# Kernel optimization log

Hardware: AMD Instinct MI355X
Metric: run time of the kernel (lower is better)

The kernel has to match this reference:

```python
import jax, jax.numpy as jnp
import numpy as np

B_J0 = 0.01   # baseline threshold
DT = 1.0
BETA = 1.8    # adaptation strength
LENS = 0.5
SCALE = 6.0
HIGHT = 0.15
GAMMA = 0.5


def _gauss(x, mu, sigma):
    return jnp.exp(-(x - mu) ** 2 / (2.0 * sigma ** 2)) / jnp.sqrt(2.0 * jnp.pi) / sigma


@jax.custom_vjp
def spike_fn(x):
    return (x > 0).astype(x.dtype)


def _spike_fwd(x):
    return spike_fn(x), x


def _spike_bwd(x, g):
    # multi-gaussian surrogate gradient (config.gradient_type == 'MG')
    temp = (_gauss(x, 0.0, LENS) * (1.0 + HIGHT)
            - _gauss(x, LENS, SCALE * LENS) * HIGHT
            - _gauss(x, -LENS, SCALE * LENS) * HIGHT)
    return (g * temp * GAMMA,)


spike_fn.defvjp(_spike_fwd, _spike_bwd)


def setup_inputs() -> dict:
    key = jax.random.key(0)
    ks = jax.random.split(key, 20)
    Bt, T, I, H, O = 256, 250, 700, 128, 20
    f32 = jnp.float32
    return {
        'x': jax.random.uniform(ks[0], (Bt, T, I), dtype=f32),
        'mask': jnp.ones((2, H, H), dtype=f32),
        'w_ih1': (jax.random.normal(ks[1], (I, H), dtype=f32) / np.sqrt(I).astype(np.float32)),
        'b_ih1': jnp.zeros((H,), f32),
        'w_h1h1': (jax.random.normal(ks[2], (H, H), dtype=f32) / np.sqrt(H).astype(np.float32)),
        'b_h1h1': jnp.zeros((H,), f32),
        'w_h1h2': (jax.random.normal(ks[3], (H, H), dtype=f32) / np.sqrt(H).astype(np.float32)),
        'b_h1h2': jnp.zeros((H,), f32),
        'w_h2h2': (jax.random.normal(ks[4], (H, H), dtype=f32) / np.sqrt(H).astype(np.float32)),
        'b_h2h2': jnp.zeros((H,), f32),
        'w_h2o': (jax.random.normal(ks[5], (H, O), dtype=f32) / np.sqrt(H).astype(np.float32)),
        'b_h2o': jnp.zeros((O,), f32),
        'tau_adp_h1': 150.0 + 10.0 * jax.random.normal(ks[6], (H,), dtype=f32),
        'tau_adp_h2': 150.0 + 10.0 * jax.random.normal(ks[7], (H,), dtype=f32),
        'tau_m_h1': 20.0 + 5.0 * jax.random.normal(ks[8], (H,), dtype=f32),
        'tau_m_h2': 20.0 + 5.0 * jax.random.normal(ks[9], (H,), dtype=f32),
        'tau_m_o': 20.0 + 5.0 * jax.random.normal(ks[10], (O,), dtype=f32),
        'hid1_mem0': jax.random.uniform(ks[11], (Bt, H), dtype=f32),
        'hid2_mem0': jax.random.uniform(ks[12], (Bt, H), dtype=f32),
        'out_mem0': jax.random.uniform(ks[13], (Bt, O), dtype=f32),
    }


def _forward(x, mask, w_ih1, b_ih1, w_h1h1, b_h1h1, w_h1h2, b_h1h2,
             w_h2h2, b_h2h2, w_h2o, b_h2o, tau_adp_h1, tau_adp_h2,
             tau_m_h1, tau_m_h2, tau_m_o, hid1_mem0, hid2_mem0, out_mem0):
    Bt, T, _ = x.shape
    H = w_ih1.shape[1]
    O = w_h2o.shape[1]
    # dropout mask applied to recurrent weights (weights stored [in, out])
    w11 = w_h1h1 * mask[0]
    w22 = w_h2h2 * mask[1]
    a1 = jnp.exp(-DT / tau_m_h1)
    r1 = jnp.exp(-DT / tau_adp_h1)
    a2 = jnp.exp(-DT / tau_m_h2)
    r2 = jnp.exp(-DT / tau_adp_h2)
    ao = jnp.exp(-DT / tau_m_o)
    # precompute input projection for all timesteps: [T, B, H]
    xin = jnp.einsum('bti,ih->tbh', x, w_ih1) + b_ih1

    def step(carry, inps):
        h1m, h1s, h2m, h2s, om, b1, b2, acc, s1, s2 = carry
        xt, t = inps
        # layer 1 (adaptive LIF)
        i1 = xt + h1s @ w11 + b_h1h1
        b1 = r1 * b1 + (1.0 - r1) * h1s
        B1 = B_J0 + BETA * b1
        h1m = h1m * a1 + (1.0 - a1) * i1 - B1 * h1s * DT
        h1s = spike_fn(h1m - B1)
        s1 = s1 + h1s
        # layer 2 (adaptive LIF)
        i2 = h1s @ w_h1h2 + b_h1h2 + h2s @ w22 + b_h2h2
        b2 = r2 * b2 + (1.0 - r2) * h2s
        B2 = B_J0 + BETA * b2
        h2m = h2m * a2 + (1.0 - a2) * i2 - B2 * h2s * DT
        h2s = spike_fn(h2m - B2)
        s2 = s2 + h2s
        # leaky-integrator readout (no spike)
        io = h2s @ w_h2o + b_h2o
        om = om * ao + (1.0 - ao) * io
        acc = acc + jnp.where(t > 10, jax.nn.softmax(om, axis=-1), 0.0)
        return (h1m, h1s, h2m, h2s, om, b1, b2, acc, s1, s2), None

    zH = jnp.zeros((Bt, H), x.dtype)
    carry0 = (hid1_mem0, zH, hid2_mem0, zH, out_mem0,
              jnp.full((Bt, H), B_J0, x.dtype), jnp.full((Bt, H), B_J0, x.dtype),
              jnp.zeros((Bt, O), x.dtype), zH, zH)
    carry, _ = jax.lax.scan(step, carry0, (xin, jnp.arange(T)))
    output, s1, s2 = carry[7], carry[8], carry[9]
    A_norm = jnp.sum(jnp.abs(w11)) + jnp.sum(jnp.abs(w22))
    return output, s1 / T, s2 / T, A_norm


def reference(x, mask, w_ih1, b_ih1, w_h1h1, b_h1h1, w_h1h2, b_h1h2,
              w_h2h2, b_h2h2, w_h2o, b_h2o, tau_adp_h1, tau_adp_h2,
              tau_m_h1, tau_m_h2, tau_m_o, hid1_mem0, hid2_mem0, out_mem0):
    return _forward(x, mask, w_ih1, b_ih1, w_h1h1, b_h1h1, w_h1h2, b_h1h2,
                    w_h2h2, b_h2h2, w_h2o, b_h2o, tau_adp_h1, tau_adp_h2,
                    tau_m_h1, tau_m_h2, tau_m_o, hid1_mem0, hid2_mem0, out_mem0)
```

## Files before the change

kernel.cpp:

```cpp
#include <hip/hip_runtime.h>
#include <math.h>

#define TT 250
#define BT 256
#define HN 128
#define ON 20
#define KIN 700
#define NKT 22

#define XIN_OFF 0
#define WPKH_OFF 8192000
#define WPKL_OFF 8237056

typedef __attribute__((ext_vector_type(8))) short bf16x8;
typedef __attribute__((ext_vector_type(4))) float f32x4;

__device__ __forceinline__ unsigned short bf16rne(float f) {
    unsigned u = __float_as_uint(f);
    unsigned r = u + 0x7fffu + ((u >> 16) & 1u);
    return (unsigned short)(r >> 16);
}
__device__ __forceinline__ void hilo(float v, short& h, short& l) {
    unsigned short hh = bf16rne(v);
    float vh = __uint_as_float((unsigned)hh << 16);
    h = (short)hh;
    l = (short)bf16rne(v - vh);
}

__device__ __forceinline__ void gl_lds16(const void* g, void* l) {
    __builtin_amdgcn_global_load_lds(
        (const __attribute__((address_space(1))) unsigned int*)g,
        (__attribute__((address_space(3))) unsigned int*)l, 16, 0, 0);
}

__global__ __launch_bounds__(256) void packw(const float* __restrict__ w,
                                             unsigned short* __restrict__ ph,
                                             unsigned short* __restrict__ pl) {
    int i = blockIdx.x * 256 + threadIdx.x;
    int k = i >> 7, c = i & 127;
    float v = (k < KIN) ? w[k * HN + c] : 0.f;
    short h, l;
    hilo(v, h, l);
    int dst = (((k >> 5) * 8 + (c >> 4)) * 64 + (((k >> 3) & 3) * 16 + (c & 15))) * 8 + (k & 7);
    ph[dst] = (unsigned short)h;
    pl[dst] = (unsigned short)l;
}

__device__ __forceinline__ void stage_kt(const unsigned short* __restrict__ wph,
                                         const unsigned short* __restrict__ wpl,
                                         void* buf, int kt, int tid) {
    const char* sh = (const char*)wph + kt * 8192 + tid * 16;
    const char* sl = (const char*)wpl + kt * 8192 + tid * 16;
    char* b = (char*)buf;
    const int wb = (tid >> 6) * 1024;
    gl_lds16(sh,        b + wb);
    gl_lds16(sh + 4096, b + wb + 4096);
    gl_lds16(sl,        b + wb + 8192);
    gl_lds16(sl + 4096, b + wb + 12288);
}

__device__ __forceinline__ void loadx8(float* av, const float* p, bool tailq3) {
    *(float4*)&av[0] = *(const float4*)p;
    if (tailq3) {
        av[4] = 0.f; av[5] = 0.f; av[6] = 0.f; av[7] = 0.f;
    } else {
        *(float4*)&av[4] = *(const float4*)(p + 4);
    }
}

__global__ __launch_bounds__(256, 2) void gemm_in(const float* __restrict__ x,
        const unsigned short* __restrict__ wph, const unsigned short* __restrict__ wpl,
        const float* __restrict__ bias1, const float* __restrict__ bias2,
        float* __restrict__ xin) {
    __shared__ __align__(16) unsigned char wbuf[2][16384];
    const int tid = threadIdx.x;
    const int w = tid >> 6, lane = tid & 63;
    const int q = lane >> 4, li = lane & 15;
    const long mbase = (long)blockIdx.x * 128;
    const float* xr0 = x + (mbase + w * 16 + li) * KIN + q * 8;

    f32x4 acc[2][8];
#pragma unroll
    for (int c = 0; c < 2; c++)
#pragma unroll
        for (int nt = 0; nt < 8; nt++) acc[c][nt] = (f32x4){0.f, 0.f, 0.f, 0.f};

    stage_kt(wph, wpl, wbuf[0], 0, tid);
    float av[2][8];
    loadx8(av[0], xr0, false);
    loadx8(av[1], xr0 + 64 * KIN, false);
    __syncthreads();

    for (int kt = 0; kt < NKT; kt++) {
        if (kt + 1 < NKT)
            stage_kt(wph, wpl, wbuf[(kt + 1) & 1], kt + 1, tid);
        const bf16x8* cv = (const bf16x8*)&wbuf[kt & 1][0];
#pragma unroll
        for (int c = 0; c < 2; c++) {
            bf16x8 ah, al;
#pragma unroll
            for (int j = 0; j < 8; j++) {
                short h, l;
                hilo(av[c][j], h, l);
                ah[j] = h; al[j] = l;
            }
            if (kt + 1 < NKT)
                loadx8(av[c], xr0 + c * (64 * KIN) + (kt + 1) * 32,
                       (kt + 1 == NKT - 1) && (q == 3));
#pragma unroll
            for (int nt = 0; nt < 8; nt++) {
                bf16x8 bh = cv[nt * 64 + lane];
                bf16x8 bl = cv[512 + nt * 64 + lane];
                acc[c][nt] = __builtin_amdgcn_mfma_f32_16x16x32_bf16(ah, bh, acc[c][nt], 0, 0, 0);
                acc[c][nt] = __builtin_amdgcn_mfma_f32_16x16x32_bf16(al, bh, acc[c][nt], 0, 0, 0);
                acc[c][nt] = __builtin_amdgcn_mfma_f32_16x16x32_bf16(ah, bl, acc[c][nt], 0, 0, 0);
            }
        }
        __syncthreads();
    }

    float b12[8];
#pragma unroll
    for (int nt = 0; nt < 8; nt++) {
        int c = nt * 16 + li;
        b12[nt] = bias1[c] + bias2[c];
    }
#pragma unroll
    for (int c = 0; c < 2; c++) {
#pragma unroll
        for (int r = 0; r < 4; r++) {
            long m = mbase + c * 64 + w * 16 + q * 4 + r;
            int bq = (int)(((unsigned long long)m * 67109ull) >> 24);
            int tt = (int)m - bq * 250;
            float* dst = xin + ((size_t)tt * BT + bq) * HN;
#pragma unroll
            for (int nt = 0; nt < 8; nt++) dst[nt * 16 + li] = acc[c][nt][r] + b12[nt];
        }
    }
}

__global__ __launch_bounds__(512, 2) void snn_scan(
    const float* __restrict__ xin, const float* __restrict__ mask,
    const float* __restrict__ w_h1h1, const float* __restrict__ w_h1h2,
    const float* __restrict__ b_h1h2, const float* __restrict__ w_h2h2,
    const float* __restrict__ b_h2h2, const float* __restrict__ w_h2o,
    const float* __restrict__ b_h2o, const float* __restrict__ tau_adp1,
    const float* __restrict__ tau_adp2, const float* __restrict__ taum1,
    const float* __restrict__ taum2, const float* __restrict__ taumo,
    const float* __restrict__ h1m0, const float* __restrict__ h2m0,
    const float* __restrict__ om0, float* __restrict__ out) {

    __shared__ __align__(16) unsigned short sA1[2 * 2048];
    __shared__ __align__(16) unsigned short sA2[2 * 2048];
    __shared__ float omb[2][16 * ON];
    __shared__ float red[8];

    const int tid = threadIdx.x;
    const int w = tid >> 6, lane = tid & 63;
    const int q = lane >> 4, li = lane & 15;
    const int col = w * 16 + li;
    const int r0 = blockIdx.x * 16;

    bf16x8 h11[4], l11[4], h22[4], l22[4], h12[4], l12[4], hO[4], lO[4];
    const int ocol = (w == 6) ? li : 16 + li;
    const bool oval = (w >= 6) && (ocol < ON);
    float pn = 0.f;
#pragma unroll
    for (int kt = 0; kt < 4; kt++) {
#pragma unroll
        for (int j = 0; j < 8; j++) {
            const int k = kt * 32 + q * 8 + j;
            const int idx = k * HN + col;
            float v11 = w_h1h1[idx] * mask[idx];
            float v22 = w_h2h2[idx] * mask[HN * HN + idx];
            float v12 = w_h1h2[idx];
            pn += fabsf(v11) + fabsf(v22);
            short hh, ll;
            hilo(v11, hh, ll); h11[kt][j] = hh; l11[kt][j] = ll;
            hilo(v22, hh, ll); h22[kt][j] = hh; l22[kt][j] = ll;
            hilo(v12, hh, ll); h12[kt][j] = hh; l12[kt][j] = ll;
            float vO = oval ? w_h2o[k * ON + ocol] : 0.f;
            hilo(vO, hh, ll); hO[kt][j] = hh; lO[kt][j] = ll;
        }
    }

    const float a1 = expf(-1.f / taum1[col]);
    const float r1 = expf(-1.f / tau_adp1[col]);
    const float a2 = expf(-1.f / taum2[col]);
    const float r2 = expf(-1.f / tau_adp2[col]);
    const float cc2 = b_h1h2[col] + b_h2h2[col];
    float h1m[4], h2m[4], b1[4], b2[4], c1[4], c2n[4];
    unsigned s1bits = 0, s2bits = 0;
#pragma unroll
    for (int r = 0; r < 4; r++) {
        h1m[r] = h1m0[(r0 + q * 4 + r) * HN + col];
        h2m[r] = h2m0[(r0 + q * 4 + r) * HN + col];
        b1[r] = 0.01f; b2[r] = 0.01f; c1[r] = 0.f; c2n[r] = 0.f;
    }
    const float ao = oval ? expf(-1.f / taumo[ocol]) : 0.f;
    const float bo = oval ? b_h2o[ocol] : 0.f;
    float om[4];
#pragma unroll
    for (int r = 0; r < 4; r++)
        om[r] = oval ? om0[(r0 + q * 4 + r) * ON + ocol] : 0.f;
    const int sm = lane >> 2, ob = (lane & 3) * 5;
    float accs[5] = {0.f, 0.f, 0.f, 0.f, 0.f};

    {
        unsigned* z1 = (unsigned*)sA1;
        unsigned* z2 = (unsigned*)sA2;
        z1[tid] = 0u; z1[tid + 512] = 0u; z1[tid + 1024] = 0u; z1[tid + 1536] = 0u;
        z2[tid] = 0u; z2[tid + 512] = 0u; z2[tid + 1024] = 0u; z2[tid + 1536] = 0u;
    }

#pragma unroll
    for (int off = 32; off > 0; off >>= 1) pn += __shfl_down(pn, off);
    if (lane == 0) red[w] = pn;
    __syncthreads();
    if (tid == 0 && blockIdx.x == 0) {
        float s = 0.f;
#pragma unroll
        for (int i = 0; i < 8; i++) s += red[i];
        out[70656] = s;
    }

    const int wbase = (w >> 1) * 512 + (((2 * w + (li >> 3)) & 3) * 16 + q * 4) * 8 + (li & 7);
    const unsigned short ONE = 0x3F80u;

    const float* xp = xin + (size_t)(r0 + q * 4) * HN + col;

    for (int i = 0; i < TT; i++) {
        const int pa = i & 1;

        float xt[4];
#pragma unroll
        for (int r = 0; r < 4; r++) xt[r] = xp[r * HN];
        xp += BT * HN;

        const bf16x8* g1p = (const bf16x8*)(sA1 + ((pa ^ 1) << 11));
        const bf16x8* f2p = (const bf16x8*)(sA2 + (pa << 11));
        bf16x8 g1[4], f2[4];
#pragma unroll
        for (int kt = 0; kt < 4; kt++) {
            g1[kt] = g1p[kt * 64 + lane];
            f2[kt] = f2p[kt * 64 + lane];
        }

        f32x4 aI = {0.f, 0.f, 0.f, 0.f}, aJ = {0.f, 0.f, 0.f, 0.f}, aG = {0.f, 0.f, 0.f, 0.f};
#pragma unroll
        for (int kt = 0; kt < 4; kt++) {
            aI = __builtin_amdgcn_mfma_f32_16x16x32_bf16(g1[kt], h11[kt], aI, 0, 0, 0);
            aI = __builtin_amdgcn_mfma_f32_16x16x32_bf16(g1[kt], l11[kt], aI, 0, 0, 0);
            aJ = __builtin_amdgcn_mfma_f32_16x16x32_bf16(g1[kt], h12[kt], aJ, 0, 0, 0);
            aJ = __builtin_amdgcn_mfma_f32_16x16x32_bf16(g1[kt], l12[kt], aJ, 0, 0, 0);
            aG = __builtin_amdgcn_mfma_f32_16x16x32_bf16(f2[kt], h22[kt], aG, 0, 0, 0);
            aG = __builtin_amdgcn_mfma_f32_16x16x32_bf16(f2[kt], l22[kt], aG, 0, 0, 0);
        }
        f32x4 aO = {0.f, 0.f, 0.f, 0.f};
        if (w >= 6) {
#pragma unroll
            for (int kt = 0; kt < 4; kt++) {
                aO = __builtin_amdgcn_mfma_f32_16x16x32_bf16(f2[kt], hO[kt], aO, 0, 0, 0);
                aO = __builtin_amdgcn_mfma_f32_16x16x32_bf16(f2[kt], lO[kt], aO, 0, 0, 0);
            }
        }

        if (i >= 1) {
            unsigned short* s2w = sA2 + ((pa ^ 1) << 11);
#pragma unroll
            for (int r = 0; r < 4; r++) {
                const float sv = (float)((s2bits >> r) & 1u);
                const float i2 = aJ[r] + aG[r] + cc2;
                b2[r] = r2 * b2[r] + (1.f - r2) * sv;
                const float B = 0.01f + 1.8f * b2[r];
                h2m[r] = a2 * h2m[r] + (1.f - a2) * i2 - B * sv;
                const bool sp = (h2m[r] - B) > 0.f;
                s2bits = sp ? (s2bits | (1u << r)) : (s2bits & ~(1u << r));
                c2n[r] += sp ? 1.f : 0.f;
                s2w[wbase + r * 8] = sp ? ONE : (unsigned short)0;
            }
        }

        if (w >= 6 && i >= 2) {
#pragma unroll
            for (int r = 0; r < 4; r++) {
                om[r] = ao * om[r] + (1.f - ao) * (bo + aO[r]);
                if (oval) omb[pa][(q * 4 + r) * ON + ocol] = om[r];
            }
        }

        if (w == 0 && i >= 14) {
            float v[5], e[5];
            float mx = -1e30f;
#pragma unroll
            for (int s = 0; s < 5; s++) { v[s] = omb[pa ^ 1][sm * ON + ob + s]; mx = fmaxf(mx, v[s]); }
            mx = fmaxf(mx, __shfl_xor(mx, 1));
            mx = fmaxf(mx, __shfl_xor(mx, 2));
            float se = 0.f;
#pragma unroll
            for (int s = 0; s < 5; s++) { e[s] = __expf(v[s] - mx); se += e[s]; }
            se += __shfl_xor(se, 1);
            se += __shfl_xor(se, 2);
            const float inv = 1.f / se;
#pragma unroll
            for (int s = 0; s < 5; s++) accs[s] += e[s] * inv;
        }

        {
            unsigned short* s1w = sA1 + (pa << 11);
#pragma unroll
            for (int r = 0; r < 4; r++) {
                const float sv = (float)((s1bits >> r) & 1u);
                const float i1 = xt[r] + aI[r];
                b1[r] = r1 * b1[r] + (1.f - r1) * sv;
                const float B = 0.01f + 1.8f * b1[r];
                h1m[r] = a1 * h1m[r] + (1.f - a1) * i1 - B * sv;
                const bool sp = (h1m[r] - B) > 0.f;
                s1bits = sp ? (s1bits | (1u << r)) : (s1bits & ~(1u << r));
                c1[r] += sp ? 1.f : 0.f;
                s1w[wbase + r * 8] = sp ? ONE : (unsigned short)0;
            }
        }
        __syncthreads();
    }

    {
        const bf16x8* g1p = (const bf16x8*)(sA1 + 2048);
        const bf16x8* f2p = (const bf16x8*)(sA2);
        bf16x8 g1[4], f2[4];
#pragma unroll
        for (int kt = 0; kt < 4; kt++) {
            g1[kt] = g1p[kt * 64 + lane];
            f2[kt] = f2p[kt * 64 + lane];
        }
        f32x4 aJ = {0.f, 0.f, 0.f, 0.f}, aG = {0.f, 0.f, 0.f, 0.f};
#pragma unroll
        for (int kt = 0; kt < 4; kt++) {
            aJ = __builtin_amdgcn_mfma_f32_16x16x32_bf16(g1[kt], h12[kt], aJ, 0, 0, 0);
            aJ = __builtin_amdgcn_mfma_f32_16x16x32_bf16(g1[kt], l12[kt], aJ, 0, 0, 0);
            aG = __builtin_amdgcn_mfma_f32_16x16x32_bf16(f2[kt], h22[kt], aG, 0, 0, 0);
            aG = __builtin_amdgcn_mfma_f32_16x16x32_bf16(f2[kt], l22[kt], aG, 0, 0, 0);
        }
        f32x4 aO = {0.f, 0.f, 0.f, 0.f};
        if (w >= 6) {
#pragma unroll
            for (int kt = 0; kt < 4; kt++) {
                aO = __builtin_amdgcn_mfma_f32_16x16x32_bf16(f2[kt], hO[kt], aO, 0, 0, 0);
                aO = __builtin_amdgcn_mfma_f32_16x16x32_bf16(f2[kt], lO[kt], aO, 0, 0, 0);
            }
        }
        {
            unsigned short* s2w = sA2 + 2048;
#pragma unroll
            for (int r = 0; r < 4; r++) {
                const float sv = (float)((s2bits >> r) & 1u);
                const float i2 = aJ[r] + aG[r] + cc2;
                b2[r] = r2 * b2[r] + (1.f - r2) * sv;
                const float B = 0.01f + 1.8f * b2[r];
                h2m[r] = a2 * h2m[r] + (1.f - a2) * i2 - B * sv;
                const bool sp = (h2m[r] - B) > 0.f;
                s2bits = sp ? (s2bits | (1u << r)) : (s2bits & ~(1u << r));
                c2n[r] += sp ? 1.f : 0.f;
                s2w[wbase + r * 8] = sp ? ONE : (unsigned short)0;
            }
        }
        if (w >= 6) {
#pragma unroll
            for (int r = 0; r < 4; r++) {
                om[r] = ao * om[r] + (1.f - ao) * (bo + aO[r]);
                if (oval) omb[0][(q * 4 + r) * ON + ocol] = om[r];
            }
        }
        if (w == 0) {
            float v[5], e[5];
            float mx = -1e30f;
#pragma unroll
            for (int s = 0; s < 5; s++) { v[s] = omb[1][sm * ON + ob + s]; mx = fmaxf(mx, v[s]); }
            mx = fmaxf(mx, __shfl_xor(mx, 1));
            mx = fmaxf(mx, __shfl_xor(mx, 2));
            float se = 0.f;
#pragma unroll
            for (int s = 0; s < 5; s++) { e[s] = __expf(v[s] - mx); se += e[s]; }
            se += __shfl_xor(se, 1);
            se += __shfl_xor(se, 2);
            const float inv = 1.f / se;
#pragma unroll
            for (int s = 0; s < 5; s++) accs[s] += e[s] * inv;
        }
        __syncthreads();
    }
    {
        if (w >= 6) {
            const bf16x8* f2p = (const bf16x8*)(sA2 + 2048);
            bf16x8 f2[4];
#pragma unroll
            for (int kt = 0; kt < 4; kt++) f2[kt] = f2p[kt * 64 + lane];
            f32x4 aO = {0.f, 0.f, 0.f, 0.f};
#pragma unroll
            for (int kt = 0; kt < 4; kt++) {
                aO = __builtin_amdgcn_mfma_f32_16x16x32_bf16(f2[kt], hO[kt], aO, 0, 0, 0);
                aO = __builtin_amdgcn_mfma_f32_16x16x32_bf16(f2[kt], lO[kt], aO, 0, 0, 0);
            }
#pragma unroll
            for (int r = 0; r < 4; r++) {
                om[r] = ao * om[r] + (1.f - ao) * (bo + aO[r]);
                if (oval) omb[1][(q * 4 + r) * ON + ocol] = om[r];
            }
        }
        if (w == 0) {
            float v[5], e[5];
            float mx = -1e30f;
#pragma unroll
            for (int s = 0; s < 5; s++) { v[s] = omb[0][sm * ON + ob + s]; mx = fmaxf(mx, v[s]); }
            mx = fmaxf(mx, __shfl_xor(mx, 1));
            mx = fmaxf(mx, __shfl_xor(mx, 2));
            float se = 0.f;
#pragma unroll
            for (int s = 0; s < 5; s++) { e[s] = __expf(v[s] - mx); se += e[s]; }
            se += __shfl_xor(se, 1);
            se += __shfl_xor(se, 2);
            const float inv = 1.f / se;
#pragma unroll
            for (int s = 0; s < 5; s++) accs[s] += e[s] * inv;
        }
        __syncthreads();
    }
    if (w == 0) {
        float v[5], e[5];
        float mx = -1e30f;
#pragma unroll
        for (int s = 0; s < 5; s++) { v[s] = omb[1][sm * ON + ob + s]; mx = fmaxf(mx, v[s]); }
        mx = fmaxf(mx, __shfl_xor(mx, 1));
        mx = fmaxf(mx, __shfl_xor(mx, 2));
        float se = 0.f;
#pragma unroll
        for (int s = 0; s < 5; s++) { e[s] = __expf(v[s] - mx); se += e[s]; }
        se += __shfl_xor(se, 1);
        se += __shfl_xor(se, 2);
        const float inv = 1.f / se;
#pragma unroll
        for (int s = 0; s < 5; s++) out[(r0 + sm) * ON + ob + s] = accs[s] + e[s] * inv;
    }
#pragma unroll
    for (int r = 0; r < 4; r++) {
        out[5120 + (r0 + q * 4 + r) * HN + col] = c1[r] * (1.f / 250.f);
        out[37888 + (r0 + q * 4 + r) * HN + col] = c2n[r] * (1.f / 250.f);
    }
}

extern "C" void kernel_launch(void* const* d_in, const int* in_sizes, int n_in,
                              void* d_out, int out_size, void* d_ws, size_t ws_size,
                              hipStream_t stream) {
    const float* x        = (const float*)d_in[0];
    const float* mask     = (const float*)d_in[1];
    const float* w_ih1    = (const float*)d_in[2];
    const float* b_ih1    = (const float*)d_in[3];
    const float* w_h1h1   = (const float*)d_in[4];
    const float* b_h1h1   = (const float*)d_in[5];
    const float* w_h1h2   = (const float*)d_in[6];
    const float* b_h1h2   = (const float*)d_in[7];
    const float* w_h2h2   = (const float*)d_in[8];
    const float* b_h2h2   = (const float*)d_in[9];
    const float* w_h2o    = (const float*)d_in[10];
    const float* b_h2o    = (const float*)d_in[11];
    const float* tau_adp1 = (const float*)d_in[12];
    const float* tau_adp2 = (const float*)d_in[13];
    const float* taum1    = (const float*)d_in[14];
    const float* taum2    = (const float*)d_in[15];
    const float* taumo    = (const float*)d_in[16];
    const float* h1m0     = (const float*)d_in[17];
    const float* h2m0     = (const float*)d_in[18];
    const float* om0      = (const float*)d_in[19];
    float* out = (float*)d_out;
    float* ws  = (float*)d_ws;

    float* xin = ws + XIN_OFF;
    unsigned short* wph = (unsigned short*)(ws + WPKH_OFF);
    unsigned short* wpl = (unsigned short*)(ws + WPKL_OFF);

    packw<<<352, 256, 0, stream>>>(w_ih1, wph, wpl);
    gemm_in<<<500, 256, 0, stream>>>(x, wph, wpl, b_ih1, b_h1h1, xin);
    snn_scan<<<16, 512, 0, stream>>>(xin, mask, w_h1h1, w_h1h2, b_h1h2, w_h2h2,
                                     b_h2h2, w_h2o, b_h2o, tau_adp1, tau_adp2,
                                     taum1, taum2, taumo, h1m0, h2m0, om0, out);
}
```

Baseline: 559.1 us.

## Stage x tiles through swizzled LDS in input GEMM; move low-half recurrent weights to LDS

The input-projection GEMM now runs 512 threads per block, each wave owning one 16-row slab, and it streams x tiles into double-buffered, XOR-swizzled shared memory with async global-to-LDS loads instead of per-thread register loads. This is meant to improve load coalescing and overlap. Separately, the scan kernel keeps the low-order bf16 halves of the recurrent and readout weights in shared memory rather than registers and reorders the MFMA groups. That cuts register pressure in the serial time loop at the cost of extra LDS reads each step.

Measured after the change: 577.6 us. 3.3% more time.

```diff
diff --git a/kernel.cpp b/kernel.cpp
--- a/kernel.cpp
+++ b/kernel.cpp
@@ -46,75 +46,72 @@
     pl[dst] = (unsigned short)l;
 }
 
-__device__ __forceinline__ void stage_kt(const unsigned short* __restrict__ wph,
-                                         const unsigned short* __restrict__ wpl,
-                                         void* buf, int kt, int tid) {
-    const char* sh = (const char*)wph + kt * 8192 + tid * 16;
-    const char* sl = (const char*)wpl + kt * 8192 + tid * 16;
-    char* b = (char*)buf;
-    const int wb = (tid >> 6) * 1024;
-    gl_lds16(sh,        b + wb);
-    gl_lds16(sh + 4096, b + wb + 4096);
-    gl_lds16(sl,        b + wb + 8192);
-    gl_lds16(sl + 4096, b + wb + 12288);
-}
-
-__device__ __forceinline__ void loadx8(float* av, const float* p, bool tailq3) {
-    *(float4*)&av[0] = *(const float4*)p;
-    if (tailq3) {
-        av[4] = 0.f; av[5] = 0.f; av[6] = 0.f; av[7] = 0.f;
-    } else {
-        *(float4*)&av[4] = *(const float4*)(p + 4);
-    }
-}
-
-__global__ __launch_bounds__(256, 2) void gemm_in(const float* __restrict__ x,
+__global__ __launch_bounds__(512, 2) void gemm_in(const float* __restrict__ x,
         const unsigned short* __restrict__ wph, const unsigned short* __restrict__ wpl,
         const float* __restrict__ bias1, const float* __restrict__ bias2,
         float* __restrict__ xin) {
     __shared__ __align__(16) unsigned char wbuf[2][16384];
+    __shared__ __align__(16) unsigned char xbuf[2][16384];
     const int tid = threadIdx.x;
     const int w = tid >> 6, lane = tid & 63;
     const int q = lane >> 4, li = lane & 15;
     const long mbase = (long)blockIdx.x * 128;
-    const float* xr0 = x + (mbase + w * 16 + li) * KIN + q * 8;
-
-    f32x4 acc[2][8];
-#pragma unroll
-    for (int c = 0; c < 2; c++)
-#pragma unroll
-        for (int nt = 0; nt < 8; nt++) acc[c][nt] = (f32x4){0.f, 0.f, 0.f, 0.f};
-
-    stage_kt(wph, wpl, wbuf[0], 0, tid);
-    float av[2][8];
-    loadx8(av[0], xr0, false);
-    loadx8(av[1], xr0 + 64 * KIN, false);
+
+    const int xrow1 = tid >> 3;
+    const int xrow2 = xrow1 + 64;
+    const int xcs1 = (tid & 7) ^ (xrow1 & 7);
+    const int xcs2 = (tid & 7) ^ (xrow2 & 7);
+    const int wbase = w * 1024;
+
+    f32x4 acc[8];
+#pragma unroll
+    for (int nt = 0; nt < 8; nt++) acc[nt] = (f32x4){0.f, 0.f, 0.f, 0.f};
+
+    auto stage = [&](int kt, int buf) {
+        char* wb = (char*)wbuf[buf];
+        char* xb = (char*)xbuf[buf];
+        gl_lds16((const char*)wph + kt * 8192 + tid * 16, wb + wbase);
+        gl_lds16((const char*)wpl + kt * 8192 + tid * 16, wb + 8192 + wbase);
+        int c1 = xcs1, c2 = xcs2;
+        if (kt == NKT - 1) {
+            if (c1 == 7) c1 = 6;
+            if (c2 == 7) c2 = 6;
+        }
+        gl_lds16((const char*)x + (mbase + xrow1) * (KIN * 4) + kt * 128 + c1 * 16,
+                 xb + wbase);
+        gl_lds16((const char*)x + (mbase + xrow2) * (KIN * 4) + kt * 128 + c2 * 16,
+                 xb + 8192 + wbase);
+    };
+
+    stage(0, 0);
     __syncthreads();
 
+    const int xaddr = (w * 16 + li) * 128 + ((q * 32) ^ ((li & 7) << 4));
+
     for (int kt = 0; kt < NKT; kt++) {
-        if (kt + 1 < NKT)
-            stage_kt(wph, wpl, wbuf[(kt + 1) & 1], kt + 1, tid);
+        if (kt + 1 < NKT) stage(kt + 1, (kt + 1) & 1);
+
+        const char* xc = (const char*)xbuf[kt & 1];
+        float av[8];
+        *(float4*)&av[0] = *(const float4*)(xc + xaddr);
+        *(float4*)&av[4] = *(const float4*)(xc + (xaddr ^ 16));
+
+        bf16x8 ah, al;
+#pragma unroll
+        for (int j = 0; j < 8; j++) {
+            short h, l;
+            hilo(av[j], h, l);
+            ah[j] = h; al[j] = l;
+        }
+
         const bf16x8* cv = (const bf16x8*)&wbuf[kt & 1][0];
 #pragma unroll
-        for (int c = 0; c < 2; c++) {
-            bf16x8 ah, al;
-#pragma unroll
-            for (int j = 0; j < 8; j++) {
-                short h, l;
-                hilo(av[c][j], h, l);
-                ah[j] = h; al[j] = l;
-            }
-            if (kt + 1 < NKT)
-                loadx8(av[c], xr0 + c * (64 * KIN) + (kt + 1) * 32,
-                       (kt + 1 == NKT - 1) && (q == 3));
-#pragma unroll
-            for (int nt = 0; nt < 8; nt++) {
-                bf16x8 bh = cv[nt * 64 + lane];
-                bf16x8 bl = cv[512 + nt * 64 + lane];
-                acc[c][nt] = __builtin_amdgcn_mfma_f32_16x16x32_bf16(ah, bh, acc[c][nt], 0, 0, 0);
-                acc[c][nt] = __builtin_amdgcn_mfma_f32_16x16x32_bf16(al, bh, acc[c][nt], 0, 0, 0);
-                acc[c][nt] = __builtin_amdgcn_mfma_f32_16x16x32_bf16(ah, bl, acc[c][nt], 0, 0, 0);
-            }
+        for (int nt = 0; nt < 8; nt++) {
+            bf16x8 bh = cv[nt * 64 + lane];
+            bf16x8 bl = cv[512 + nt * 64 + lane];
+            acc[nt] = __builtin_amdgcn_mfma_f32_16x16x32_bf16(ah, bh, acc[nt], 0, 0, 0);
+            acc[nt] = __builtin_amdgcn_mfma_f32_16x16x32_bf16(al, bh, acc[nt], 0, 0, 0);
+            acc[nt] = __builtin_amdgcn_mfma_f32_16x16x32_bf16(ah, bl, acc[nt], 0, 0, 0);
         }
         __syncthreads();
     }
@@ -126,16 +123,13 @@
         b12[nt] = bias1[c] + bias2[c];
     }
 #pragma unroll
-    for (int c = 0; c < 2; c++) {
-#pragma unroll
-        for (int r = 0; r < 4; r++) {
-            long m = mbase + c * 64 + w * 16 + q * 4 + r;
-            int bq = (int)(((unsigned long long)m * 67109ull) >> 24);
-            int tt = (int)m - bq * 250;
-            float* dst = xin + ((size_t)tt * BT + bq) * HN;
-#pragma unroll
-            for (int nt = 0; nt < 8; nt++) dst[nt * 16 + li] = acc[c][nt][r] + b12[nt];
-        }
+    for (int r = 0; r < 4; r++) {
+        long m = mbase + w * 16 + q * 4 + r;
+        int bq = (int)(((unsigned long long)m * 67109ull) >> 24);
+        int tt = (int)m - bq * 250;
+        float* dst = xin + ((size_t)tt * BT + bq) * HN;
+#pragma unroll
+        for (int nt = 0; nt < 8; nt++) dst[nt * 16 + li] = acc[nt][r] + b12[nt];
     }
 }
 
@@ -152,6 +146,8 @@
 
     __shared__ __align__(16) unsigned short sA1[2 * 2048];
     __shared__ __align__(16) unsigned short sA2[2 * 2048];
+    __shared__ __align__(16) unsigned short sloW[8 * 3 * 4 * 64 * 8];
+    __shared__ __align__(16) unsigned short sloO[2 * 4 * 64 * 8];
     __shared__ float omb[2][16 * ON];
     __shared__ float red[8];
 
@@ -161,12 +157,17 @@
     const int col = w * 16 + li;
     const int r0 = blockIdx.x * 16;
 
-    bf16x8 h11[4], l11[4], h22[4], l22[4], h12[4], l12[4], hO[4], lO[4];
+    bf16x8 h11[4], h22[4], h12[4], hO[4];
     const int ocol = (w == 6) ? li : 16 + li;
     const bool oval = (w >= 6) && (ocol < ON);
+    bf16x8* lo11w = (bf16x8*)sloW + w * 768;
+    bf16x8* lo22w = lo11w + 256;
+    bf16x8* lo12w = lo11w + 512;
+    bf16x8* loOw  = (bf16x8*)sloO + ((w >= 6) ? (w - 6) * 256 : 0);
     float pn = 0.f;
 #pragma unroll
     for (int kt = 0; kt < 4; kt++) {
+        bf16x8 L11, L22, L12, LO;
 #pragma unroll
         for (int j = 0; j < 8; j++) {
             const int k = kt * 32 + q * 8 + j;
@@ -176,12 +177,16 @@
             float v12 = w_h1h2[idx];
             pn += fabsf(v11) + fabsf(v22);
             short hh, ll;
-            hilo(v11, hh, ll); h11[kt][j] = hh; l11[kt][j] = ll;
-            hilo(v22, hh, ll); h22[kt][j] = hh; l22[kt][j] = ll;
-            hilo(v12, hh, ll); h12[kt][j] = hh; l12[kt][j] = ll;
+            hilo(v11, hh, ll); h11[kt][j] = hh; L11[j] = ll;
+            hilo(v22, hh, ll); h22[kt][j] = hh; L22[j] = ll;
+            hilo(v12, hh, ll); h12[kt][j] = hh; L12[j] = ll;
             float vO = oval ? w_h2o[k * ON + ocol] : 0.f;
-            hilo(vO, hh, ll); hO[kt][j] = hh; lO[kt][j] = ll;
-        }
+            hilo(vO, hh, ll); hO[kt][j] = hh; LO[j] = ll;
+        }
+        lo11w[kt * 64 + lane] = L11;
+        lo22w[kt * 64 + lane] = L22;
+        lo12w[kt * 64 + lane] = L12;
+        if (w >= 6) loOw[kt * 64 + lane] = LO;
     }
 
     const float a1 = expf(-1.f / taum1[col]);
@@ -227,6 +232,11 @@
     const int wbase = (w >> 1) * 512 + (((2 * w + (li >> 3)) & 3) * 16 + q * 4) * 8 + (li & 7);
     const unsigned short ONE = 0x3F80u;
 
+    const bf16x8* lo11r = (const bf16x8*)sloW + w * 768;
+    const bf16x8* lo22r = lo11r + 256;
+    const bf16x8* lo12r = lo11r + 512;
+    const bf16x8* loOr  = (const bf16x8*)sloO + ((w >= 6) ? (w - 6) * 256 : 0);
+
     const float* xp = xin + (size_t)(r0 + q * 4) * HN + col;
 
     for (int i = 0; i < TT; i++) {
@@ -246,22 +256,42 @@
             f2[kt] = f2p[kt * 64 + lane];
         }
 
-        f32x4 aI = {0.f, 0.f, 0.f, 0.f}, aJ = {0.f, 0.f, 0.f, 0.f}, aG = {0.f, 0.f, 0.f, 0.f};
-#pragma unroll
-        for (int kt = 0; kt < 4; kt++) {
-            aI = __builtin_amdgcn_mfma_f32_16x16x32_bf16(g1[kt], h11[kt], aI, 0, 0, 0);
-            aI = __builtin_amdgcn_mfma_f32_16x16x32_bf16(g1[kt], l11[kt], aI, 0, 0, 0);
-            aJ = __builtin_amdgcn_mfma_f32_16x16x32_bf16(g1[kt], h12[kt], aJ, 0, 0, 0);
-            aJ = __builtin_amdgcn_mfma_f32_16x16x32_bf16(g1[kt], l12[kt], aJ, 0, 0, 0);
-            aG = __builtin_amdgcn_mfma_f32_16x16x32_bf16(f2[kt], h22[kt], aG, 0, 0, 0);
-            aG = __builtin_amdgcn_mfma_f32_16x16x32_bf16(f2[kt], l22[kt], aG, 0, 0, 0);
+        f32x4 aJ = {0.f, 0.f, 0.f, 0.f}, aG = {0.f, 0.f, 0.f, 0.f};
+        {
+            bf16x8 t12[4], t22[4];
+#pragma unroll
+            for (int kt = 0; kt < 4; kt++) {
+                t12[kt] = lo12r[kt * 64 + lane];
+                t22[kt] = lo22r[kt * 64 + lane];
+            }
+#pragma unroll
+            for (int kt = 0; kt < 4; kt++) {
+                aJ = __builtin_amdgcn_mfma_f32_16x16x32_bf16(g1[kt], h12[kt], aJ, 0, 0, 0);
+                aJ = __builtin_amdgcn_mfma_f32_16x16x32_bf16(g1[kt], t12[kt], aJ, 0, 0, 0);
+                aG = __builtin_amdgcn_mfma_f32_16x16x32_bf16(f2[kt], h22[kt], aG, 0, 0, 0);
+                aG = __builtin_amdgcn_mfma_f32_16x16x32_bf16(f2[kt], t22[kt], aG, 0, 0, 0);
+            }
         }
         f32x4 aO = {0.f, 0.f, 0.f, 0.f};
         if (w >= 6) {
+            bf16x8 tO[4];
+#pragma unroll
+            for (int kt = 0; kt < 4; kt++) tO[kt] = loOr[kt * 64 + lane];
 #pragma unroll
             for (int kt = 0; kt < 4; kt++) {
                 aO = __builtin_amdgcn_mfma_f32_16x16x32_bf16(f2[kt], hO[kt], aO, 0, 0, 0);
-                aO = __builtin_amdgcn_mfma_f32_16x16x32_bf16(f2[kt], lO[kt], aO, 0, 0, 0);
+                aO = __builtin_amdgcn_mfma_f32_16x16x32_bf16(f2[kt], tO[kt], aO, 0, 0, 0);
+            }
+        }
+        f32x4 aI = {0.f, 0.f, 0.f, 0.f};
+        {
+            bf16x8 t11[4];
+#pragma unroll
+            for (int kt = 0; kt < 4; kt++) t11[kt] = lo11r[kt * 64 + lane];
+#pragma unroll
+            for (int kt = 0; kt < 4; kt++) {
+                aI = __builtin_amdgcn_mfma_f32_16x16x32_bf16(g1[kt], h11[kt], aI, 0, 0, 0);
+                aI = __builtin_amdgcn_mfma_f32_16x16x32_bf16(g1[kt], t11[kt], aI, 0, 0, 0);
             }
         }
 
@@ -327,26 +357,31 @@
     {
         const bf16x8* g1p = (const bf16x8*)(sA1 + 2048);
         const bf16x8* f2p = (const bf16x8*)(sA2);
-        bf16x8 g1[4], f2[4];
+        bf16x8 g1[4], f2[4], t12[4], t22[4];
 #pragma unroll
         for (int kt = 0; kt < 4; kt++) {
             g1[kt] = g1p[kt * 64 + lane];
             f2[kt] = f2p[kt * 64 + lane];
+            t12[kt] = lo12r[kt * 64 + lane];
+            t22[kt] = lo22r[kt * 64 + lane];
         }
         f32x4 aJ = {0.f, 0.f, 0.f, 0.f}, aG = {0.f, 0.f, 0.f, 0.f};
 #pragma unroll
         for (int kt = 0; kt < 4; kt++) {
             aJ = __builtin_amdgcn_mfma_f32_16x16x32_bf16(g1[kt], h12[kt], aJ, 0, 0, 0);
-            aJ = __builtin_amdgcn_mfma_f32_16x16x32_bf16(g1[kt], l12[kt], aJ, 0, 0, 0);
+            aJ = __builtin_amdgcn_mfma_f32_16x16x32_bf16(g1[kt], t12[kt], aJ, 0, 0, 0);
             aG = __builtin_amdgcn_mfma_f32_16x16x32_bf16(f2[kt], h22[kt], aG, 0, 0, 0);
-            aG = __builtin_amdgcn_mfma_f32_16x16x32_bf16(f2[kt], l22[kt], aG, 0, 0, 0);
+            aG = __builtin_amdgcn_mfma_f32_16x16x32_bf16(f2[kt], t22[kt], aG, 0, 0, 0);
         }
         f32x4 aO = {0.f, 0.f, 0.f, 0.f};
         if (w >= 6) {
+            bf16x8 tO[4];
+#pragma unroll
+            for (int kt = 0; kt < 4; kt++) tO[kt] = loOr[kt * 64 + lane];
 #pragma unroll
             for (int kt = 0; kt < 4; kt++) {
                 aO = __builtin_amdgcn_mfma_f32_16x16x32_bf16(f2[kt], hO[kt], aO, 0, 0, 0);
-                aO = __builtin_amdgcn_mfma_f32_16x16x32_bf16(f2[kt], lO[kt], aO, 0, 0, 0);
+                aO = __builtin_amdgcn_mfma_f32_16x16x32_bf16(f2[kt], tO[kt], aO, 0, 0, 0);
             }
         }
         {
@@ -392,14 +427,17 @@
     {
         if (w >= 6) {
             const bf16x8* f2p = (const bf16x8*)(sA2 + 2048);
-            bf16x8 f2[4];
-#pragma unroll
-            for (int kt = 0; kt < 4; kt++) f2[kt] = f2p[kt * 64 + lane];
+            bf16x8 f2[4], tO[4];
+#pragma unroll
+            for (int kt = 0; kt < 4; kt++) {
+                f2[kt] = f2p[kt * 64 + lane];
+                tO[kt] = loOr[kt * 64 + lane];
+            }
             f32x4 aO = {0.f, 0.f, 0.f, 0.f};
 #pragma unroll
             for (int kt = 0; kt < 4; kt++) {
                 aO = __builtin_amdgcn_mfma_f32_16x16x32_bf16(f2[kt], hO[kt], aO, 0, 0, 0);
-                aO = __builtin_amdgcn_mfma_f32_16x16x32_bf16(f2[kt], lO[kt], aO, 0, 0, 0);
+                aO = __builtin_amdgcn_mfma_f32_16x16x32_bf16(f2[kt], tO[kt], aO, 0, 0, 0);
             }
 #pragma unroll
             for (int r = 0; r < 4; r++) {
@@ -479,7 +517,7 @@
     unsigned short* wpl = (unsigned short*)(ws + WPKL_OFF);
 
     packw<<<352, 256, 0, stream>>>(w_ih1, wph, wpl);
-    gemm_in<<<500, 256, 0, stream>>>(x, wph, wpl, b_ih1, b_h1h1, xin);
+    gemm_in<<<500, 512, 0, stream>>>(x, wph, wpl, b_ih1, b_h1h1, xin);
     snn_scan<<<16, 512, 0, stream>>>(xin, mask, w_h1h1, w_h1h2, b_h1h2, w_h2h2,
                                      b_h2h2, w_h2o, b_h2o, tau_adp1, tau_adp2,
                                      taum1, taum2, taumo, h1m0, h2m0, om0, out);
```
